# Kernel optimization log

Hardware: AMD Instinct MI355X
Metric: run time of the kernel (lower is better)

Reference implementation:

```python
import math
import jax, jax.numpy as jnp
import numpy as np

LOG2PI = math.log(2.0 * math.pi)


def _log_density_sum(mean, logvar, sample):
    # Gaussian log-density, summed over the trailing feature dim.
    # mean/logvar/sample broadcast against each other.
    inv_sigma = jnp.exp(-logvar)
    tmp = (sample - mean) * inv_sigma
    return jnp.sum(-0.5 * (tmp * tmp + 2.0 * logvar + LOG2PI), axis=-1)


def setup_inputs() -> dict:
    key = jax.random.key(0)
    ks = jax.random.split(key, 6)
    B, T, DF, DZ = 128, 32, 256, 128
    return {
        "f_mean":   jax.random.normal(ks[0], (B, DF), dtype=jnp.float32),
        "f_logvar": jax.random.normal(ks[1], (B, DF), dtype=jnp.float32),
        "f_sample": jax.random.normal(ks[2], (B, DF), dtype=jnp.float32),
        "z_mean":   jax.random.normal(ks[3], (B, T, DZ), dtype=jnp.float32),
        "z_logvar": jax.random.normal(ks[4], (B, T, DZ), dtype=jnp.float32),
        "z_sample": jax.random.normal(ks[5], (B, T, DZ), dtype=jnp.float32),
        "num_train": 50000,
    }


def reference(f_mean, f_logvar, f_sample, z_mean, z_logvar, z_sample, num_train):
    B = f_mean.shape[0]
    log_norm = math.log(B) + math.log(num_train)

    # f pairwise: sample index i vs mean index j -> [B_i, B_j]
    # (original repeats this identically over every step t)
    logq_f_sum = _log_density_sum(
        f_mean[None, :, :], f_logvar[None, :, :], f_sample[:, None, :]
    )  # [B, B]

    # z pairwise per step: transpose to [T, B, D], then [T, B_i, B_j]
    zt_mean = jnp.transpose(z_mean, (1, 0, 2))
    zt_logvar = jnp.transpose(z_logvar, (1, 0, 2))
    zt_sample = jnp.transpose(z_sample, (1, 0, 2))
    logq_z_sum = _log_density_sum(
        zt_mean[:, None, :, :], zt_logvar[:, None, :, :], zt_sample[:, :, None, :]
    )  # [T, B, B]

    # concatenating f and z components along the feature dim then summing
    # equals summing the per-component feature sums
    logq_fz_sum = logq_f_sum[None, :, :] + logq_z_sum  # [T, B, B]

    logq_f = jax.nn.logsumexp(logq_f_sum, axis=1) - log_norm          # [B]
    logq_z = jax.nn.logsumexp(logq_z_sum, axis=2) - log_norm          # [T, B]
    logq_fz = jax.nn.logsumexp(logq_fz_sum, axis=2) - log_norm        # [T, B]

    mi_fz = jnp.mean(jax.nn.relu(logq_fz - logq_f[None, :] - logq_z))
    return mi_fz
```

## Files before the change

### kernel.cpp

```cpp
#include <hip/hip_runtime.h>

#define LOG2PI 1.8378770664093453f



__device__ __forceinline__ float waveReduceSum(float v) {
#pragma unroll
    for (int o = 32; o > 0; o >>= 1) v += __shfl_down(v, o, 64);
    return v;
}

__device__ __forceinline__ float waveReduceMax(float v) {
#pragma unroll
    for (int o = 32; o > 0; o >>= 1) v = fmaxf(v, __shfl_down(v, o, 64));
    return v;
}

__device__ __forceinline__ float blockReduceSum(float v, float* sh) {
    int lane = threadIdx.x & 63, wid = threadIdx.x >> 6, nw = blockDim.x >> 6;
    v = waveReduceSum(v);
    __syncthreads();
    if (lane == 0) sh[wid] = v;
    __syncthreads();
    float r = sh[0];
    for (int w = 1; w < nw; ++w) r += sh[w];
    return r;
}

__device__ __forceinline__ float blockReduceMax(float v, float* sh) {
    int lane = threadIdx.x & 63, wid = threadIdx.x >> 6, nw = blockDim.x >> 6;
    v = waveReduceMax(v);
    __syncthreads();
    if (lane == 0) sh[wid] = v;
    __syncthreads();
    float r = sh[0];
    for (int w = 1; w < nw; ++w) r = fmaxf(r, sh[w]);
    return r;
}

__device__ __forceinline__ float4 blockMax4(float4 v, float4* sh) {
#pragma unroll
    for (int o = 32; o > 0; o >>= 1) {
        v.x = fmaxf(v.x, __shfl_down(v.x, o, 64));
        v.y = fmaxf(v.y, __shfl_down(v.y, o, 64));
        v.z = fmaxf(v.z, __shfl_down(v.z, o, 64));
        v.w = fmaxf(v.w, __shfl_down(v.w, o, 64));
    }
    int lane = threadIdx.x & 63, wid = threadIdx.x >> 6;
    __syncthreads();
    if (lane == 0) sh[wid] = v;
    __syncthreads();
    float4 a = sh[0], b = sh[1];
    return make_float4(fmaxf(a.x, b.x), fmaxf(a.y, b.y),
                       fmaxf(a.z, b.z), fmaxf(a.w, b.w));
}

__device__ __forceinline__ float4 blockSum4(float4 v, float4* sh) {
#pragma unroll
    for (int o = 32; o > 0; o >>= 1) {
        v.x += __shfl_down(v.x, o, 64);
        v.y += __shfl_down(v.y, o, 64);
        v.z += __shfl_down(v.z, o, 64);
        v.w += __shfl_down(v.w, o, 64);
    }
    int lane = threadIdx.x & 63, wid = threadIdx.x >> 6;
    __syncthreads();
    if (lane == 0) sh[wid] = v;
    __syncthreads();
    float4 a = sh[0], b = sh[1];
    return make_float4(a.x + b.x, a.y + b.y, a.z + b.z, a.w + b.w);
}

#define NB_TZ 512
#define NB_TF 32
#define NB_ZS 2048
#define NB_FS 128

__global__ void prep(const float* __restrict__ zm, const float* __restrict__ zlv,
                     const float* __restrict__ fm, const float* __restrict__ flv,
                     float2* __restrict__ zme, float2* __restrict__ fme,
                     float* __restrict__ cz, float* __restrict__ cf,
                     float* __restrict__ out) {
    __shared__ float S[2 * 32 * 33];
    float (*sm)[33] = (float(*)[33])S;
    float (*se)[33] = (float(*)[33])(S + 32 * 33);
    int blk = blockIdx.x;
    int tid = threadIdx.x;

    if (blk < NB_TZ) {
        int t = blk >> 4, bt = (blk >> 2) & 3, dt = blk & 3;
        int tx = tid & 31, ty = tid >> 5;
        int b0 = bt * 32, d0 = dt * 32;
#pragma unroll
        for (int k = 0; k < 4; ++k) {
            int bl = ty + k * 8;
            int idx = (b0 + bl) * 4096 + t * 128 + d0 + tx;
            sm[bl][tx] = zm[idx];
            se[bl][tx] = expf(-2.f * zlv[idx]);
        }
        __syncthreads();
#pragma unroll
        for (int k = 0; k < 4; ++k) {
            int dl = ty + k * 8;
            zme[(t * 128 + d0 + dl) * 128 + b0 + tx] =
                make_float2(sm[tx][dl], se[tx][dl]);
        }
    } else if (blk < NB_TZ + NB_TF) {
        int r = blk - NB_TZ;
        int bt = r >> 3, dt = r & 7;
        int tx = tid & 31, ty = tid >> 5;
        int b0 = bt * 32, d0 = dt * 32;
#pragma unroll
        for (int k = 0; k < 4; ++k) {
            int bl = ty + k * 8;
            int idx = (b0 + bl) * 256 + d0 + tx;
            sm[bl][tx] = fm[idx];
            se[bl][tx] = expf(-2.f * flv[idx]);
        }
        __syncthreads();
#pragma unroll
        for (int k = 0; k < 4; ++k) {
            int dl = ty + k * 8;
            fme[(d0 + dl) * 128 + b0 + tx] = make_float2(sm[tx][dl], se[tx][dl]);
        }
    } else if (blk < NB_TZ + NB_TF + NB_ZS) {
        int r0 = (blk - NB_TZ - NB_TF) * 2;
        int half = tid >> 7, lane = tid & 127;
        int r = r0 + half;
        int b = r >> 5, t = r & 31;
        float v = 2.f * zlv[b * 4096 + t * 128 + lane];
        v = waveReduceSum(v);
        int wid = tid >> 6;
        if ((tid & 63) == 0) S[wid] = v;
        __syncthreads();
        if (tid == 0)   cz[(r0 & 31) * 128 + (r0 >> 5)] = S[0] + S[1];
        if (tid == 128) { int r1 = r0 + 1; cz[(r1 & 31) * 128 + (r1 >> 5)] = S[2] + S[3]; }
    } else if (blk < NB_TZ + NB_TF + NB_ZS + NB_FS) {
        int b = blk - NB_TZ - NB_TF - NB_ZS;
        float v = 2.f * flv[b * 256 + tid];
        v = blockReduceSum(v, S);
        if (tid == 0) cf[b] = v;
    } else {
        if (tid == 0) out[0] = 0.f;
    }
}

__global__ void fker(const float* __restrict__ fs, const float2* __restrict__ fme,
                     const float* __restrict__ cf,
                     float* __restrict__ F, float* __restrict__ lse_f) {
    __shared__ float s_fs[256];
    __shared__ float part[256];
    __shared__ float sh[4];
    int i = blockIdx.x, tid = threadIdx.x;
    int j = tid & 127, dh = tid >> 7;
    s_fs[tid] = fs[i * 256 + tid];
    __syncthreads();
    const float2* fp = fme + dh * 128 * 128;
    const float* ss = s_fs + dh * 128;
    float acc = 0.f;
#pragma unroll 8
    for (int d = 0; d < 128; ++d) {
        float2 me = fp[d * 128 + j];
        float df = ss[d] - me.x;
        acc = fmaf(df * df, me.y, acc);
    }
    part[tid] = acc;
    __syncthreads();
    float Fij = 0.f;
    if (dh == 0) {
        Fij = -0.5f * (acc + part[tid + 128] + cf[j] + 256.f * LOG2PI);
        F[i * 128 + j] = Fij;
    }
    float v = (dh == 0) ? Fij : -INFINITY;
    float m = blockReduceMax(v, sh);
    float e = (dh == 0) ? expf(Fij - m) : 0.f;
    float s = blockReduceSum(e, sh);
    if (tid == 0) lse_f[i] = m + logf(s);
}

__global__ void zker(const float* __restrict__ zs, const float2* __restrict__ zme,
                     const float* __restrict__ cz, const float* __restrict__ F,
                     const float* __restrict__ lse_f, const int* __restrict__ num_train,
                     float* __restrict__ out) {
    __shared__ float4 s_zs[128];
    __shared__ float4 sh4[2];
    int blk = blockIdx.x;
    int t = blk >> 5;
    int i0 = (blk & 31) * 4;
    int j = threadIdx.x;

    float* s_zs_f = (float*)s_zs;
#pragma unroll
    for (int k = 0; k < 4; ++k)
        s_zs_f[j * 4 + k] = zs[(i0 + k) * 4096 + t * 128 + j];
    __syncthreads();

    const float2* zmt = zme + t * 16384;
    float4 acc = make_float4(0.f, 0.f, 0.f, 0.f);
#pragma unroll 8
    for (int d = 0; d < 128; ++d) {
        float2 me = zmt[d * 128 + j];
        float4 z = s_zs[d];
        float d0 = z.x - me.x; acc.x = fmaf(d0 * d0, me.y, acc.x);
        float d1 = z.y - me.x; acc.y = fmaf(d1 * d1, me.y, acc.y);
        float d2 = z.z - me.x; acc.z = fmaf(d2 * d2, me.y, acc.z);
        float d3 = z.w - me.x; acc.w = fmaf(d3 * d3, me.y, acc.w);
    }

    float base = -0.5f * (cz[t * 128 + j] + 128.f * LOG2PI);
    float4 rz = make_float4(-0.5f * acc.x + base, -0.5f * acc.y + base,
                            -0.5f * acc.z + base, -0.5f * acc.w + base);
    float4 fz = make_float4(rz.x + F[(i0 + 0) * 128 + j],
                            rz.y + F[(i0 + 1) * 128 + j],
                            rz.z + F[(i0 + 2) * 128 + j],
                            rz.w + F[(i0 + 3) * 128 + j]);

    float4 mz = blockMax4(rz, sh4);
    float4 e = make_float4(expf(rz.x - mz.x), expf(rz.y - mz.y),
                           expf(rz.z - mz.z), expf(rz.w - mz.w));
    float4 sz = blockSum4(e, sh4);
    float4 mf = blockMax4(fz, sh4);
    e = make_float4(expf(fz.x - mf.x), expf(fz.y - mf.y),
                    expf(fz.z - mf.z), expf(fz.w - mf.w));
    float4 sf = blockSum4(e, sh4);

    if (j == 0) {
        float log_norm = logf(128.f * (float)num_train[0]);
        float lz[4] = {mz.x + logf(sz.x), mz.y + logf(sz.y),
                       mz.z + logf(sz.z), mz.w + logf(sz.w)};
        float lfz[4] = {mf.x + logf(sf.x), mf.y + logf(sf.y),
                        mf.z + logf(sf.z), mf.w + logf(sf.w)};
        float s = 0.f;
#pragma unroll
        for (int k = 0; k < 4; ++k) {
            float v = lfz[k] - lse_f[i0 + k] - lz[k] + log_norm;
            s += (v > 0.f ? v : 0.f);
        }
        atomicAdd(out, s * (1.f / 4096.f));
    }
}

extern "C" void kernel_launch(void* const* d_in, const int* in_sizes, int n_in,
                              void* d_out, int out_size, void* d_ws, size_t ws_size,
                              hipStream_t stream) {
    const float* f_mean    = (const float*)d_in[0];
    const float* f_logvar  = (const float*)d_in[1];
    const float* f_sample  = (const float*)d_in[2];
    const float* z_mean    = (const float*)d_in[3];
    const float* z_logvar  = (const float*)d_in[4];
    const float* z_sample  = (const float*)d_in[5];
    const int*   num_train = (const int*)d_in[6];
    float* out = (float*)d_out;

    float* ws    = (float*)d_ws;
    float2* zme  = (float2*)ws;
    float2* fme  = (float2*)(ws + 1048576);
    float*  cz   = ws + 1048576 + 65536;
    float*  cf   = cz + 4096;
    float*  F    = cf + 128;
    float*  lse_f= F + 16384;

    prep<<<NB_TZ + NB_TF + NB_ZS + NB_FS + 1, 256, 0, stream>>>(
        z_mean, z_logvar, f_mean, f_logvar, zme, fme, cz, cf, out);
    fker<<<128, 256, 0, stream>>>(f_sample, fme, cf, F, lse_f);
    zker<<<1024, 128, 0, stream>>>(z_sample, zme, cz, F, lse_f, num_train, out);
}
```

Measured before the change: 105.6 us.

## Process eight sample rows per zker block with split-D halves

zker now handles 8 sample rows per block instead of 4, so each zme element load is reused across twice as many rows. It uses 256 threads that split the feature dimension into two halves, combined through shared memory, and each 128-thread half then runs the logsumexp for 4 rows. The block order is remapped so adjacent blocks share t values, which may help L2 locality. In exchange there are half as many blocks, extra shared memory and one more barrier.

```diff
diff --git a/kernel.cpp b/kernel.cpp
--- a/kernel.cpp
+++ b/kernel.cpp
@@ -38,7 +38,7 @@
     return r;
 }
 
-__device__ __forceinline__ float4 blockMax4(float4 v, float4* sh) {
+__device__ __forceinline__ float4 halfMax4(float4 v, float4* sh) {
 #pragma unroll
     for (int o = 32; o > 0; o >>= 1) {
         v.x = fmaxf(v.x, __shfl_down(v.x, o, 64));
@@ -46,16 +46,17 @@
         v.z = fmaxf(v.z, __shfl_down(v.z, o, 64));
         v.w = fmaxf(v.w, __shfl_down(v.w, o, 64));
     }
-    int lane = threadIdx.x & 63, wid = threadIdx.x >> 6;
-    __syncthreads();
-    if (lane == 0) sh[wid] = v;
-    __syncthreads();
-    float4 a = sh[0], b = sh[1];
+    int wid = threadIdx.x >> 6;
+    __syncthreads();
+    if ((threadIdx.x & 63) == 0) sh[wid] = v;
+    __syncthreads();
+    int hb = (threadIdx.x >> 7) << 1;
+    float4 a = sh[hb], b = sh[hb + 1];
     return make_float4(fmaxf(a.x, b.x), fmaxf(a.y, b.y),
                        fmaxf(a.z, b.z), fmaxf(a.w, b.w));
 }
 
-__device__ __forceinline__ float4 blockSum4(float4 v, float4* sh) {
+__device__ __forceinline__ float4 halfSum4(float4 v, float4* sh) {
 #pragma unroll
     for (int o = 32; o > 0; o >>= 1) {
         v.x += __shfl_down(v.x, o, 64);
@@ -63,11 +64,12 @@
         v.z += __shfl_down(v.z, o, 64);
         v.w += __shfl_down(v.w, o, 64);
     }
-    int lane = threadIdx.x & 63, wid = threadIdx.x >> 6;
-    __syncthreads();
-    if (lane == 0) sh[wid] = v;
-    __syncthreads();
-    float4 a = sh[0], b = sh[1];
+    int wid = threadIdx.x >> 6;
+    __syncthreads();
+    if ((threadIdx.x & 63) == 0) sh[wid] = v;
+    __syncthreads();
+    int hb = (threadIdx.x >> 7) << 1;
+    float4 a = sh[hb], b = sh[hb + 1];
     return make_float4(a.x + b.x, a.y + b.y, a.z + b.z, a.w + b.w);
 }
 
@@ -182,47 +184,64 @@
                      const float* __restrict__ cz, const float* __restrict__ F,
                      const float* __restrict__ lse_f, const int* __restrict__ num_train,
                      float* __restrict__ out) {
-    __shared__ float4 s_zs[128];
-    __shared__ float4 sh4[2];
-    int blk = blockIdx.x;
-    int t = blk >> 5;
-    int i0 = (blk & 31) * 4;
-    int j = threadIdx.x;
-
-    float* s_zs_f = (float*)s_zs;
-#pragma unroll
-    for (int k = 0; k < 4; ++k)
-        s_zs_f[j * 4 + k] = zs[(i0 + k) * 4096 + t * 128 + j];
-    __syncthreads();
-
-    const float2* zmt = zme + t * 16384;
-    float4 acc = make_float4(0.f, 0.f, 0.f, 0.f);
+    __shared__ float s_zs[128 * 8];
+    __shared__ float s_acc[2][8][128];
+    __shared__ float4 sh4[4];
+    int b = blockIdx.x;
+    int t = (b & 7) + ((b >> 7) << 3);
+    int i0 = ((b >> 3) & 15) * 8;
+    int tid = threadIdx.x;
+    int j = tid & 127, h = tid >> 7;
+
+#pragma unroll
+    for (int kk = 0; kk < 4; ++kk) {
+        int k = h * 4 + kk;
+        s_zs[j * 8 + k] = zs[(i0 + k) * 4096 + t * 128 + j];
+    }
+    __syncthreads();
+
+    const float2* zp = zme + t * 16384 + h * 64 * 128;
+    float acc[8] = {0.f, 0.f, 0.f, 0.f, 0.f, 0.f, 0.f, 0.f};
 #pragma unroll 8
-    for (int d = 0; d < 128; ++d) {
-        float2 me = zmt[d * 128 + j];
-        float4 z = s_zs[d];
-        float d0 = z.x - me.x; acc.x = fmaf(d0 * d0, me.y, acc.x);
-        float d1 = z.y - me.x; acc.y = fmaf(d1 * d1, me.y, acc.y);
-        float d2 = z.z - me.x; acc.z = fmaf(d2 * d2, me.y, acc.z);
-        float d3 = z.w - me.x; acc.w = fmaf(d3 * d3, me.y, acc.w);
-    }
-
+    for (int dd = 0; dd < 64; ++dd) {
+        float2 me = zp[dd * 128 + j];
+        int d = (h << 6) + dd;
+        float4 za = *(const float4*)&s_zs[d * 8];
+        float4 zb = *(const float4*)&s_zs[d * 8 + 4];
+        float t0;
+        t0 = za.x - me.x; acc[0] = fmaf(t0 * t0, me.y, acc[0]);
+        t0 = za.y - me.x; acc[1] = fmaf(t0 * t0, me.y, acc[1]);
+        t0 = za.z - me.x; acc[2] = fmaf(t0 * t0, me.y, acc[2]);
+        t0 = za.w - me.x; acc[3] = fmaf(t0 * t0, me.y, acc[3]);
+        t0 = zb.x - me.x; acc[4] = fmaf(t0 * t0, me.y, acc[4]);
+        t0 = zb.y - me.x; acc[5] = fmaf(t0 * t0, me.y, acc[5]);
+        t0 = zb.z - me.x; acc[6] = fmaf(t0 * t0, me.y, acc[6]);
+        t0 = zb.w - me.x; acc[7] = fmaf(t0 * t0, me.y, acc[7]);
+    }
+#pragma unroll
+    for (int k = 0; k < 8; ++k) s_acc[h][k][j] = acc[k];
+    __syncthreads();
+
+    int k0 = h * 4;
     float base = -0.5f * (cz[t * 128 + j] + 128.f * LOG2PI);
-    float4 rz = make_float4(-0.5f * acc.x + base, -0.5f * acc.y + base,
-                            -0.5f * acc.z + base, -0.5f * acc.w + base);
-    float4 fz = make_float4(rz.x + F[(i0 + 0) * 128 + j],
-                            rz.y + F[(i0 + 1) * 128 + j],
-                            rz.z + F[(i0 + 2) * 128 + j],
-                            rz.w + F[(i0 + 3) * 128 + j]);
-
-    float4 mz = blockMax4(rz, sh4);
+    float4 rz, fz;
+    rz.x = -0.5f * (s_acc[0][k0 + 0][j] + s_acc[1][k0 + 0][j]) + base;
+    rz.y = -0.5f * (s_acc[0][k0 + 1][j] + s_acc[1][k0 + 1][j]) + base;
+    rz.z = -0.5f * (s_acc[0][k0 + 2][j] + s_acc[1][k0 + 2][j]) + base;
+    rz.w = -0.5f * (s_acc[0][k0 + 3][j] + s_acc[1][k0 + 3][j]) + base;
+    fz.x = rz.x + F[(i0 + k0 + 0) * 128 + j];
+    fz.y = rz.y + F[(i0 + k0 + 1) * 128 + j];
+    fz.z = rz.z + F[(i0 + k0 + 2) * 128 + j];
+    fz.w = rz.w + F[(i0 + k0 + 3) * 128 + j];
+
+    float4 mz = halfMax4(rz, sh4);
     float4 e = make_float4(expf(rz.x - mz.x), expf(rz.y - mz.y),
                            expf(rz.z - mz.z), expf(rz.w - mz.w));
-    float4 sz = blockSum4(e, sh4);
-    float4 mf = blockMax4(fz, sh4);
+    float4 sz = halfSum4(e, sh4);
+    float4 mf = halfMax4(fz, sh4);
     e = make_float4(expf(fz.x - mf.x), expf(fz.y - mf.y),
                     expf(fz.z - mf.z), expf(fz.w - mf.w));
-    float4 sf = blockSum4(e, sh4);
+    float4 sf = halfSum4(e, sh4);
 
     if (j == 0) {
         float log_norm = logf(128.f * (float)num_train[0]);
@@ -233,7 +252,7 @@
         float s = 0.f;
 #pragma unroll
         for (int k = 0; k < 4; ++k) {
-            float v = lfz[k] - lse_f[i0 + k] - lz[k] + log_norm;
+            float v = lfz[k] - lse_f[i0 + k0 + k] - lz[k] + log_norm;
             s += (v > 0.f ? v : 0.f);
         }
         atomicAdd(out, s * (1.f / 4096.f));
@@ -263,5 +282,5 @@
     prep<<<NB_TZ + NB_TF + NB_ZS + NB_FS + 1, 256, 0, stream>>>(
         z_mean, z_logvar, f_mean, f_logvar, zme, fme, cz, cf, out);
     fker<<<128, 256, 0, stream>>>(f_sample, fme, cf, F, lse_f);
-    zker<<<1024, 128, 0, stream>>>(z_sample, zme, cz, F, lse_f, num_train, out);
-}
+    zker<<<512, 256, 0, stream>>>(z_sample, zme, cz, F, lse_f, num_train, out);
+}
```

Result: no change. 105.2 us (-0.4%).
